# Optimization experiments

Measured on AMD Instinct MI355X. Metric: run time of the kernel, lower is better.

Reference implementation:

```python
import jax, jax.numpy as jnp
import numpy as np

B, H, W, D, C = 2, 32, 32, 16, 384
HEADS = 12
WH = WW = WD = 4
NOISE = 256
EPS = 1e-5


def setup_inputs() -> dict:
    key = jax.random.key(0)
    ks = jax.random.split(key, 12)
    s = 0.02
    return {
        "x": jax.random.normal(ks[0], (B, H, W, D, C), jnp.float32),
        "x_noise": jax.random.normal(ks[1], (B, NOISE), jnp.float32),
        "ada_w": jax.random.normal(ks[2], (6 * C, NOISE), jnp.float32) * s,
        "ada_b": jax.random.normal(ks[3], (6 * C,), jnp.float32) * s,
        "qkv_w": jax.random.normal(ks[4], (3 * C, C), jnp.float32) * s,
        "qkv_b": jax.random.normal(ks[5], (3 * C,), jnp.float32) * s,
        "out_w": jax.random.normal(ks[6], (C, C), jnp.float32) * s,
        "out_b": jax.random.normal(ks[7], (C,), jnp.float32) * s,
        "mlp_w1": jax.random.normal(ks[8], (4 * C, C), jnp.float32) * s,
        "mlp_b1": jax.random.normal(ks[9], (4 * C,), jnp.float32) * s,
        "mlp_w2": jax.random.normal(ks[10], (C, 4 * C), jnp.float32) * s,
        "mlp_b2": jax.random.normal(ks[11], (C,), jnp.float32) * s,
    }


def _ln(y):
    # LayerNorm without affine (elementwise_affine=False when use_ada_ln_zero)
    m = jnp.mean(y, axis=-1, keepdims=True)
    v = jnp.mean(jnp.square(y - m), axis=-1, keepdims=True)
    return (y - m) * jax.lax.rsqrt(v + EPS)


def _mod(y, shift, scale):
    # shift/scale: [B, C] broadcast over spatial dims
    return y * (1.0 + scale[:, None, None, None, :]) + shift[:, None, None, None, :]


def _gate(y, g):
    return y * g[:, None, None, None, :]


def _window_attn(q, k, v):
    # q,k,v: [B,H,W,D,C] -> windows [nw, heads, L, hd]
    hd = C // HEADS

    def part(t):
        t = t.reshape(B, H // WH, WH, W // WW, WW, D // WD, WD, HEADS, hd)
        t = t.transpose(0, 1, 3, 5, 7, 2, 4, 6, 8)  # b h w d he wh ww wd hd
        return t.reshape(-1, HEADS, WH * WW * WD, hd)

    q, k, v = part(q), part(k), part(v)
    scores = jnp.einsum("nhlc,nhmc->nhlm", q, k) / jnp.sqrt(jnp.float32(hd))
    attn = jax.nn.softmax(scores, axis=-1)
    o = jnp.einsum("nhlm,nhmc->nhlc", attn, v)
    o = o.reshape(B, H // WH, W // WW, D // WD, HEADS, WH, WW, WD, hd)
    o = o.transpose(0, 1, 5, 2, 6, 3, 7, 4, 8)  # b h wh w ww d wd he hd
    return o.reshape(B, H, W, D, C)


def reference(x, x_noise, ada_w, ada_b, qkv_w, qkv_b, out_w, out_b,
              mlp_w1, mlp_b1, mlp_w2, mlp_b2):
    # AdaLN-Zero params
    params = jax.nn.silu(x_noise) @ ada_w.T + ada_b  # [B, 6C]
    shift1, scale1, gate1, shift2, scale2, gate2 = jnp.split(params, 6, axis=-1)

    # attention branch
    qkv = _mod(_ln(x), shift1, scale1) @ qkv_w.T + qkv_b  # [B,H,W,D,3C]
    q, k, v = jnp.split(qkv, 3, axis=-1)
    attn_out = _window_attn(q, k, v)
    x = x + _gate(attn_out @ out_w.T + out_b, gate1)

    # MLP branch
    h = _mod(_ln(x), shift2, scale2) @ mlp_w1.T + mlp_b1
    h = jax.nn.gelu(h, approximate=False) @ mlp_w2.T + mlp_b2
    return x + _gate(h, gate2)
```

## Files before the change

### kernel.cpp

```cpp
#include <hip/hip_runtime.h>
#include <math.h>

typedef __bf16 bf16;
typedef __attribute__((ext_vector_type(8))) __bf16 bf16x8;
typedef __attribute__((ext_vector_type(4))) float f32x4;

__device__ __forceinline__ bf16 f2bf(float f) {
  union { float f; unsigned u; } a; a.f = f;
  unsigned r = a.u + 0x7fffu + ((a.u >> 16) & 1u);
  union { unsigned short u; bf16 b; } o; o.u = (unsigned short)(r >> 16);
  return o.b;
}

__device__ __forceinline__ void async_load16(const void* g, void* l) {
  __builtin_amdgcn_global_load_lds(
      (const __attribute__((address_space(1))) void*)g,
      (__attribute__((address_space(3))) void*)l, 16, 0, 0);
}

__global__ void f2b_kernel(const float* __restrict__ in, bf16* __restrict__ out, int n) {
  for (int i = blockIdx.x * 256 + threadIdx.x; i < n; i += gridDim.x * 256)
    out[i] = f2bf(in[i]);
}

__global__ __launch_bounds__(256)
void ada_kernel(const float* __restrict__ xn, const float* __restrict__ aw,
                const float* __restrict__ ab, float* __restrict__ params) {
  const int wid = (blockIdx.x << 2) + (threadIdx.x >> 6);
  const int ln = threadIdx.x & 63;
  const int j = wid % 2304, b = wid / 2304;
  float s = 0.f;
#pragma unroll
  for (int e = 0; e < 4; e++) {
    int idx = ln + (e << 6);
    float x = xn[b * 256 + idx];
    s += (x / (1.f + __expf(-x))) * aw[j * 256 + idx];
  }
#pragma unroll
  for (int m = 1; m < 64; m <<= 1) s += __shfl_xor(s, m);
  if (ln == 0) params[b * 2304 + j] = s + ab[j];
}

__global__ __launch_bounds__(256)
void ln_mod_kernel(const float* __restrict__ xin, const float* __restrict__ params,
                   int so, int co, bf16* __restrict__ y) {
  const int tok = (blockIdx.x << 2) + (threadIdx.x >> 6);
  const int ln = threadIdx.x & 63;
  const float* xr = xin + (size_t)tok * 384;
  float v[6]; float s = 0.f, s2 = 0.f;
#pragma unroll
  for (int e = 0; e < 6; e++) { float x = xr[ln + (e << 6)]; v[e] = x; s += x; s2 += x * x; }
#pragma unroll
  for (int m = 1; m < 64; m <<= 1) { s += __shfl_xor(s, m); s2 += __shfl_xor(s2, m); }
  const float mean = s * (1.f / 384.f);
  const float var = s2 * (1.f / 384.f) - mean * mean;
  const float rs = rsqrtf(var + 1e-5f);
  const int b = tok >> 14;
  const float* pr = params + b * 2304;
  bf16* yr = y + (size_t)tok * 384;
#pragma unroll
  for (int e = 0; e < 6; e++) {
    int c = ln + (e << 6);
    float nv = (v[e] - mean) * rs;
    yr[c] = f2bf(nv * (1.f + pr[co + c]) + pr[so + c]);
  }
}

template<int MODE>
__global__ __launch_bounds__(256)
void gemm_bt(const bf16* __restrict__ A, const bf16* __restrict__ W,
             const float* __restrict__ bias, const float* __restrict__ gate,
             const float* __restrict__ xres, float* __restrict__ outf,
             bf16* __restrict__ outb, int M, int N, int K) {
  __shared__ __align__(16) bf16 As[3][4096];
  __shared__ __align__(16) bf16 Bs[3][4096];
  const int t = threadIdx.x;
  const int mtiles = M >> 7;
  const int bm = (blockIdx.x % mtiles) << 7;
  const int bn = (blockIdx.x / mtiles) << 7;
  const int wid = t >> 6, ln = t & 63;
  const int wr = (wid >> 1) << 6, wc = (wid & 1) << 6;
  const int lrow = ln & 15;
  const int rdoff = (((ln >> 4) ^ (lrow & 3) ^ ((lrow >> 2) & 3)) & 3) << 3;

  f32x4 acc[4][4] = {};

  const int srow = t >> 2;
  const int scol = ((((t & 3) ^ (srow & 3) ^ ((srow >> 2) & 3)) & 3) << 3);
  const bf16* ga = A + (size_t)(bm + srow) * K + scol;
  const bf16* gb = W + (size_t)(bn + srow) * K + scol;
  const size_t rowskip = (size_t)64 * K;
  const int nk = K >> 5;

#define STAGE(buf, kt) do { const int k0_ = (kt) << 5;                 \
    async_load16(ga + k0_, &As[buf][t * 8]);                           \
    async_load16(ga + k0_ + rowskip, &As[buf][2048 + t * 8]);          \
    async_load16(gb + k0_, &Bs[buf][t * 8]);                           \
    async_load16(gb + k0_ + rowskip, &Bs[buf][2048 + t * 8]); } while (0)

  STAGE(0, 0); STAGE(1, 1); STAGE(2, 2);
  int cur = 0;
  for (int tk = 0; tk < nk; ++tk) {
    if (tk + 2 < nk)      asm volatile("s_waitcnt vmcnt(8)" ::: "memory");
    else if (tk + 1 < nk) asm volatile("s_waitcnt vmcnt(4)" ::: "memory");
    else                  asm volatile("s_waitcnt vmcnt(0)" ::: "memory");
    asm volatile("s_barrier" ::: "memory");

    bf16x8 af[4], bfr[4];
#pragma unroll
    for (int i = 0; i < 4; i++)
      af[i] = *(const bf16x8*)&As[cur][(wr + i * 16 + lrow) * 32 + rdoff];
#pragma unroll
    for (int j = 0; j < 4; j++)
      bfr[j] = *(const bf16x8*)&Bs[cur][(wc + j * 16 + lrow) * 32 + rdoff];
    asm volatile("s_waitcnt lgkmcnt(0)" ::: "memory");
    __builtin_amdgcn_sched_barrier(0);
    asm volatile("s_barrier" ::: "memory");

    if (tk + 3 < nk) STAGE(cur, tk + 3);

#pragma unroll
    for (int i = 0; i < 4; i++)
#pragma unroll
      for (int j = 0; j < 4; j++)
        acc[i][j] = __builtin_amdgcn_mfma_f32_16x16x32_bf16(af[i], bfr[j], acc[i][j], 0, 0, 0);

    cur = (cur == 2) ? 0 : cur + 1;
  }
#undef STAGE

  const int lr4 = (ln >> 4) << 2;
#pragma unroll
  for (int i = 0; i < 4; i++) {
#pragma unroll
    for (int j = 0; j < 4; j++) {
      const int n = bn + wc + j * 16 + lrow;
      const float bs = bias[n];
#pragma unroll
      for (int r = 0; r < 4; r++) {
        const size_t m = (size_t)(bm + wr + i * 16 + lr4 + r);
        float v = acc[i][j][r] + bs;
        if constexpr (MODE == 0) {
          outb[m * N + n] = f2bf(v);
        } else if constexpr (MODE == 1) {
          float u = 0.7978845608f * (v + 0.044715f * v * v * v);
          float e = __expf(-2.0f * u);
          float th = (1.0f - e) / (1.0f + e);
          v = 0.5f * v * (1.0f + th);
          outb[m * N + n] = f2bf(v);
        } else {
          const float g = gate[(m >> 14) * 2304 + n];
          outf[m * (size_t)N + n] = xres[m * (size_t)N + n] + g * v;
        }
      }
    }
  }
}

__global__ __launch_bounds__(256)
void attn_kernel(const bf16* __restrict__ qkv, bf16* __restrict__ out) {
  __shared__ __align__(16) bf16 Pl[4][64][72];
  __shared__ __align__(16) bf16 Vt[4][32][72];
  const int t = threadIdx.x, wv = t >> 6, ln = t & 63;
  const int blk = blockIdx.x;
  const int win = blk / 3, hg = blk % 3;
  const int head = hg * 4 + wv;
  const int db = win & 3, wb = (win >> 2) & 7, hb = (win >> 5) & 7, b = win >> 8;
  const int base = ((b * 32 + hb * 4) * 32 + wb * 4) * 16 + db * 4;
  const int lrow = ln & 15, lk8 = (ln >> 4) << 3;
  const float scale = 0.17677669529663689f;

#define TOKROW(q) (base + ((q) >> 4) * 512 + (((q) >> 2) & 3) * 16 + ((q) & 3))

  {
    size_t rb = (size_t)TOKROW(ln) * 1152 + 768 + head * 32;
#pragma unroll
    for (int fi = 0; fi < 4; fi++) {
      bf16x8 v = *(const bf16x8*)(qkv + rb + fi * 8);
#pragma unroll
      for (int e = 0; e < 8; e++) Vt[wv][fi * 8 + e][ln] = v[e];
    }
  }

  f32x4 sacc[4][4] = {};
  {
    bf16x8 qf[4], kf[4];
#pragma unroll
    for (int mi = 0; mi < 4; mi++)
      qf[mi] = *(const bf16x8*)(qkv + (size_t)TOKROW(mi * 16 + lrow) * 1152 + head * 32 + lk8);
#pragma unroll
    for (int nj = 0; nj < 4; nj++)
      kf[nj] = *(const bf16x8*)(qkv + (size_t)TOKROW(nj * 16 + lrow) * 1152 + 384 + head * 32 + lk8);
#pragma unroll
    for (int mi = 0; mi < 4; mi++)
#pragma unroll
      for (int nj = 0; nj < 4; nj++)
        sacc[mi][nj] = __builtin_amdgcn_mfma_f32_16x16x32_bf16(qf[mi], kf[nj], sacc[mi][nj], 0, 0, 0);
  }

#pragma unroll
  for (int mi = 0; mi < 4; mi++) {
#pragma unroll
    for (int r = 0; r < 4; r++) {
      float s0 = sacc[mi][0][r] * scale, s1 = sacc[mi][1][r] * scale;
      float s2 = sacc[mi][2][r] * scale, s3 = sacc[mi][3][r] * scale;
      float mx = fmaxf(fmaxf(s0, s1), fmaxf(s2, s3));
#pragma unroll
      for (int m = 1; m < 16; m <<= 1) mx = fmaxf(mx, __shfl_xor(mx, m));
      float e0 = __expf(s0 - mx), e1 = __expf(s1 - mx), e2 = __expf(s2 - mx), e3 = __expf(s3 - mx);
      float sm = e0 + e1 + e2 + e3;
#pragma unroll
      for (int m = 1; m < 16; m <<= 1) sm += __shfl_xor(sm, m);
      const float inv = 1.0f / sm;
      const int row = mi * 16 + ((ln >> 4) << 2) + r;
      Pl[wv][row][0 + lrow]  = f2bf(e0 * inv);
      Pl[wv][row][16 + lrow] = f2bf(e1 * inv);
      Pl[wv][row][32 + lrow] = f2bf(e2 * inv);
      Pl[wv][row][48 + lrow] = f2bf(e3 * inv);
    }
  }

  f32x4 oacc[4][2] = {};
#pragma unroll
  for (int kk = 0; kk < 2; kk++) {
    bf16x8 pa[4], vb[2];
#pragma unroll
    for (int mi = 0; mi < 4; mi++) pa[mi] = *(const bf16x8*)&Pl[wv][mi * 16 + lrow][kk * 32 + lk8];
#pragma unroll
    for (int nj = 0; nj < 2; nj++) vb[nj] = *(const bf16x8*)&Vt[wv][nj * 16 + lrow][kk * 32 + lk8];
#pragma unroll
    for (int mi = 0; mi < 4; mi++)
#pragma unroll
      for (int nj = 0; nj < 2; nj++)
        oacc[mi][nj] = __builtin_amdgcn_mfma_f32_16x16x32_bf16(pa[mi], vb[nj], oacc[mi][nj], 0, 0, 0);
  }

#pragma unroll
  for (int mi = 0; mi < 4; mi++)
#pragma unroll
    for (int nj = 0; nj < 2; nj++)
#pragma unroll
      for (int r = 0; r < 4; r++) {
        int q = mi * 16 + ((ln >> 4) << 2) + r;
        out[(size_t)TOKROW(q) * 384 + head * 32 + nj * 16 + lrow] = f2bf(oacc[mi][nj][r]);
      }
#undef TOKROW
}

extern "C" void kernel_launch(void* const* d_in, const int* in_sizes, int n_in,
                              void* d_out, int out_size, void* d_ws, size_t ws_size,
                              hipStream_t stream) {
  const float* x      = (const float*)d_in[0];
  const float* xnoise = (const float*)d_in[1];
  const float* ada_w  = (const float*)d_in[2];
  const float* ada_b  = (const float*)d_in[3];
  const float* qkv_w  = (const float*)d_in[4];
  const float* qkv_b  = (const float*)d_in[5];
  const float* out_w  = (const float*)d_in[6];
  const float* out_b  = (const float*)d_in[7];
  const float* mlp_w1 = (const float*)d_in[8];
  const float* mlp_b1 = (const float*)d_in[9];
  const float* mlp_w2 = (const float*)d_in[10];
  const float* mlp_b2 = (const float*)d_in[11];
  float* out = (float*)d_out;

  char* ws = (char*)d_ws;
  float* params = (float*)(ws + 0);
  bf16* wq    = (bf16*)(ws + 18432);
  bf16* wo    = (bf16*)(ws + 903168);
  bf16* w1    = (bf16*)(ws + 1198080);
  bf16* w2    = (bf16*)(ws + 2377728);
  bf16* ybuf  = (bf16*)(ws + 3557376);
  bf16* qkvb  = (bf16*)(ws + 28723200);
  bf16* hbuf  = qkvb;

  f2b_kernel<<<1728, 256, 0, stream>>>(qkv_w, wq, 442368);
  f2b_kernel<<<576, 256, 0, stream>>>(out_w, wo, 147456);
  f2b_kernel<<<2304, 256, 0, stream>>>(mlp_w1, w1, 589824);
  f2b_kernel<<<2304, 256, 0, stream>>>(mlp_w2, w2, 589824);
  ada_kernel<<<1152, 256, 0, stream>>>(xnoise, ada_w, ada_b, params);
  ln_mod_kernel<<<8192, 256, 0, stream>>>(x, params, 0, 384, ybuf);
  gemm_bt<0><<<dim3(256 * 9), 256, 0, stream>>>(ybuf, wq, qkv_b, nullptr, nullptr, nullptr,
                                                qkvb, 32768, 1152, 384);
  attn_kernel<<<1536, 256, 0, stream>>>(qkvb, ybuf);
  gemm_bt<2><<<dim3(256 * 3), 256, 0, stream>>>(ybuf, wo, out_b, params + 2 * 384, x, out,
                                                nullptr, 32768, 384, 384);
  ln_mod_kernel<<<8192, 256, 0, stream>>>(out, params, 1152, 1536, ybuf);
  gemm_bt<1><<<dim3(256 * 12), 256, 0, stream>>>(ybuf, w1, mlp_b1, nullptr, nullptr, nullptr,
                                                 hbuf, 32768, 1536, 384);
  gemm_bt<2><<<dim3(256 * 3), 256, 0, stream>>>(hbuf, w2, mlp_b2, params + 5 * 384, out, out,
                                                nullptr, 32768, 384, 1536);

  (void)in_sizes; (void)n_in; (void)out_size; (void)ws_size;
}
```

Before: 390.9 us.

## Load GEMM weight fragments directly into registers instead of through LDS

The B (weight) operand no longer goes through shared memory. Each lane loads its MFMA fragments straight from global memory into a three-deep register ring, while A keeps the async LDS triple buffer. The k-loop is unrolled by six with hand-tuned vmcnt waits so the register ring indices stay compile-time constants. This halves LDS traffic and footprint, which may raise occupancy, but it adds register pressure and uncoalesced-ish 16-byte global loads. It also assumes nk is at least 12 and a multiple of 6, and depends on fragile vmcnt counting.

```diff
diff --git a/kernel.cpp b/kernel.cpp
--- a/kernel.cpp
+++ b/kernel.cpp
@@ -73,14 +73,13 @@
              const float* __restrict__ xres, float* __restrict__ outf,
              bf16* __restrict__ outb, int M, int N, int K) {
   __shared__ __align__(16) bf16 As[3][4096];
-  __shared__ __align__(16) bf16 Bs[3][4096];
   const int t = threadIdx.x;
   const int mtiles = M >> 7;
   const int bm = (blockIdx.x % mtiles) << 7;
   const int bn = (blockIdx.x / mtiles) << 7;
   const int wid = t >> 6, ln = t & 63;
   const int wr = (wid >> 1) << 6, wc = (wid & 1) << 6;
-  const int lrow = ln & 15;
+  const int lrow = ln & 15, lk8 = (ln >> 4) << 3;
   const int rdoff = (((ln >> 4) ^ (lrow & 3) ^ ((lrow >> 2) & 3)) & 3) << 3;
 
   f32x4 acc[4][4] = {};
@@ -88,46 +87,70 @@
   const int srow = t >> 2;
   const int scol = ((((t & 3) ^ (srow & 3) ^ ((srow >> 2) & 3)) & 3) << 3);
   const bf16* ga = A + (size_t)(bm + srow) * K + scol;
-  const bf16* gb = W + (size_t)(bn + srow) * K + scol;
   const size_t rowskip = (size_t)64 * K;
+  const bf16* gw = W + (size_t)(bn + wc + lrow) * K + lk8;
   const int nk = K >> 5;
 
-#define STAGE(buf, kt) do { const int k0_ = (kt) << 5;                 \
+  bf16x8 bb[3][4];
+
+#define STAGEA(buf, kt) do { const int k0_ = (kt) << 5;                \
     async_load16(ga + k0_, &As[buf][t * 8]);                           \
-    async_load16(ga + k0_ + rowskip, &As[buf][2048 + t * 8]);          \
-    async_load16(gb + k0_, &Bs[buf][t * 8]);                           \
-    async_load16(gb + k0_ + rowskip, &Bs[buf][2048 + t * 8]); } while (0)
-
-  STAGE(0, 0); STAGE(1, 1); STAGE(2, 2);
-  int cur = 0;
-  for (int tk = 0; tk < nk; ++tk) {
-    if (tk + 2 < nk)      asm volatile("s_waitcnt vmcnt(8)" ::: "memory");
-    else if (tk + 1 < nk) asm volatile("s_waitcnt vmcnt(4)" ::: "memory");
-    else                  asm volatile("s_waitcnt vmcnt(0)" ::: "memory");
-    asm volatile("s_barrier" ::: "memory");
-
-    bf16x8 af[4], bfr[4];
-#pragma unroll
-    for (int i = 0; i < 4; i++)
-      af[i] = *(const bf16x8*)&As[cur][(wr + i * 16 + lrow) * 32 + rdoff];
-#pragma unroll
-    for (int j = 0; j < 4; j++)
-      bfr[j] = *(const bf16x8*)&Bs[cur][(wc + j * 16 + lrow) * 32 + rdoff];
-    asm volatile("s_waitcnt lgkmcnt(0)" ::: "memory");
-    __builtin_amdgcn_sched_barrier(0);
-    asm volatile("s_barrier" ::: "memory");
-
-    if (tk + 3 < nk) STAGE(cur, tk + 3);
-
-#pragma unroll
-    for (int i = 0; i < 4; i++)
-#pragma unroll
-      for (int j = 0; j < 4; j++)
-        acc[i][j] = __builtin_amdgcn_mfma_f32_16x16x32_bf16(af[i], bfr[j], acc[i][j], 0, 0, 0);
-
-    cur = (cur == 2) ? 0 : cur + 1;
-  }
-#undef STAGE
+    async_load16(ga + k0_ + rowskip, &As[buf][2048 + t * 8]); } while (0)
+
+  STAGEA(0, 0); STAGEA(1, 1); STAGEA(2, 2);
+  __builtin_amdgcn_sched_barrier(0);
+#pragma unroll
+  for (int j = 0; j < 4; j++) bb[0][j] = *(const bf16x8*)(gw + (size_t)j * 16 * K);
+#pragma unroll
+  for (int j = 0; j < 4; j++) bb[1][j] = *(const bf16x8*)(gw + (size_t)j * 16 * K + 32);
+  __builtin_amdgcn_sched_barrier(0);
+
+#define BODY(TK, R, RL, NW, DOSTAGE, DOLOADB)                                  \
+  {                                                                            \
+    asm volatile("s_waitcnt vmcnt(" NW ")" ::: "memory");                      \
+    asm volatile("s_barrier" ::: "memory");                                    \
+    bf16x8 af[4];                                                              \
+    _Pragma("unroll") for (int i = 0; i < 4; i++)                              \
+      af[i] = *(const bf16x8*)&As[R][(wr + i * 16 + lrow) * 32 + rdoff];       \
+    asm volatile("s_waitcnt lgkmcnt(0)" ::: "memory");                         \
+    __builtin_amdgcn_sched_barrier(0);                                         \
+    asm volatile("s_barrier" ::: "memory");                                    \
+    if (DOLOADB) {                                                             \
+      _Pragma("unroll") for (int j = 0; j < 4; j++)                            \
+        bb[RL][j] = *(const bf16x8*)(gw + (size_t)j * 16 * K + (((TK) + 2) << 5)); \
+      __builtin_amdgcn_sched_barrier(0);                                       \
+    }                                                                          \
+    if (DOSTAGE) { STAGEA(R, (TK) + 3); __builtin_amdgcn_sched_barrier(0); }   \
+    _Pragma("unroll") for (int i = 0; i < 4; i++)                              \
+      _Pragma("unroll") for (int j = 0; j < 4; j++)                            \
+        acc[i][j] = __builtin_amdgcn_mfma_f32_16x16x32_bf16(af[i], bb[R][j], acc[i][j], 0, 0, 0); \
+  }
+
+  BODY(0, 0, 2, "12", true, true);
+  BODY(1, 1, 0, "16", true, true);
+  BODY(2, 2, 1, "20", true, true);
+  BODY(3, 0, 2, "12", true, true);
+  BODY(4, 1, 0, "12", true, true);
+  BODY(5, 2, 1, "12", true, true);
+  for (int tk0 = 6; tk0 + 6 < nk; tk0 += 6) {
+    BODY(tk0 + 0, 0, 2, "12", true, true);
+    BODY(tk0 + 1, 1, 0, "12", true, true);
+    BODY(tk0 + 2, 2, 1, "12", true, true);
+    BODY(tk0 + 3, 0, 2, "12", true, true);
+    BODY(tk0 + 4, 1, 0, "12", true, true);
+    BODY(tk0 + 5, 2, 1, "12", true, true);
+  }
+  {
+    const int tn = nk - 6;
+    BODY(tn + 0, 0, 2, "12", true, true);
+    BODY(tn + 1, 1, 0, "12", true, true);
+    BODY(tn + 2, 2, 1, "12", true, true);
+    BODY(tn + 3, 0, 2, "12", false, true);
+    BODY(tn + 4, 1, 0, "10", false, false);
+    BODY(tn + 5, 2, 1, "4",  false, false);
+  }
+#undef BODY
+#undef STAGEA
 
   const int lr4 = (ln >> 4) << 2;
 #pragma unroll
```

Measured after the change: 483.7 us. +23.7%, slower.
